# Performance work log

Measured on AMD Instinct MI355X. Metric: run time of the kernel, lower is better.

The kernel has to match this reference:

```python
import jax, jax.numpy as jnp
import numpy as np

B, S, HID = 2, 2048, 1024
H, HKV, D = 8, 2, 256
G = H // HKV            # GQA group size = 4
RD = D // 4             # partial rotary dim = 64
BASE = 10000000.0
EPS = 1e-6


def _rmsnorm(x, w):
    # x: [..., D]; matches QwenRMSNorm (fp32 math)
    xf = x.astype(jnp.float32)
    var = jnp.mean(xf * xf, axis=-1, keepdims=True)
    return w * (xf * jax.lax.rsqrt(var + EPS)).astype(x.dtype)


def _rotate_half(x):
    h = x.shape[-1] // 2
    return jnp.concatenate([-x[..., h:], x[..., :h]], axis=-1)


def _rope_cos_sin(position_ids, dtype):
    inv_freq = 1.0 / (BASE ** (jnp.arange(0, RD, 2, dtype=jnp.float32) / RD))
    freqs = position_ids.astype(jnp.float32)[:, None] * inv_freq[None, :]  # [S, RD/2]
    emb = jnp.concatenate([freqs, freqs], axis=-1)                          # [S, RD]
    return jnp.cos(emb).astype(dtype)[None, None], jnp.sin(emb).astype(dtype)[None, None]


def setup_inputs() -> dict:
    key = jax.random.key(0)
    ks = jax.random.split(key, 8)
    sc = lambda fan_in: 1.0 / np.sqrt(fan_in)
    return {
        "hidden_states": jax.random.normal(ks[0], (B, S, HID), jnp.float32),
        "position_ids": jnp.arange(S, dtype=jnp.int32),
        "Wq": jax.random.normal(ks[1], (H * D * 2, HID), jnp.float32) * sc(HID),
        "Wk": jax.random.normal(ks[2], (HKV * D, HID), jnp.float32) * sc(HID),
        "Wv": jax.random.normal(ks[3], (HKV * D, HID), jnp.float32) * sc(HID),
        "Wo": jax.random.normal(ks[4], (HID, H * D), jnp.float32) * sc(H * D),
        "q_norm_w": jnp.ones((D,), jnp.float32),
        "k_norm_w": jnp.ones((D,), jnp.float32),
    }


def reference(hidden_states, position_ids, Wq, Wk, Wv, Wo, q_norm_w, k_norm_w):
    b, s, _ = hidden_states.shape
    q_and_gate = hidden_states @ Wq.T                      # [B,S,2*H*D]
    q = q_and_gate[..., : H * D]
    gate = q_and_gate[..., H * D :]
    k = hidden_states @ Wk.T                               # [B,S,HKV*D]
    v = hidden_states @ Wv.T

    q = _rmsnorm(q.reshape(b, s, H, D), q_norm_w).transpose(0, 2, 1, 3)    # [B,H,S,D]
    k = _rmsnorm(k.reshape(b, s, HKV, D), k_norm_w).transpose(0, 2, 1, 3)  # [B,HKV,S,D]
    v = v.reshape(b, s, HKV, D).transpose(0, 2, 1, 3)                       # [B,HKV,S,D]

    cos, sin = _rope_cos_sin(position_ids, q.dtype)        # [1,1,S,RD]
    q_rot, q_pass = q[..., :RD], q[..., RD:]
    k_rot, k_pass = k[..., :RD], k[..., RD:]
    q = jnp.concatenate([q_rot * cos + _rotate_half(q_rot) * sin, q_pass], axis=-1)
    k = jnp.concatenate([k_rot * cos + _rotate_half(k_rot) * sin, k_pass], axis=-1)

    # GQA: group q heads by kv head instead of repeat_interleave (same math)
    qg = q.reshape(b, HKV, G, s, D)
    scale = 1.0 / np.sqrt(D).astype(np.float32)
    scores = jnp.einsum('bhgqd,bhkd->bhgqk', qg, k) * scale  # [B,HKV,G,S,S]
    attn = jax.nn.softmax(scores, axis=-1)                   # NOTE: no causal mask (as in source)
    out = jnp.einsum('bhgqk,bhkd->bhgqd', attn, v)           # [B,HKV,G,S,D]
    out = out.reshape(b, H, s, D).transpose(0, 2, 1, 3).reshape(b, s, H * D)

    out = out * jax.nn.silu(gate)
    return out @ Wo.T
```

## Files before the change

kernel.cpp:

```cpp
#include <hip/hip_runtime.h>
#include <math.h>

typedef unsigned short u16;
typedef unsigned int   u32;
typedef __attribute__((ext_vector_type(4))) float f32x4;
typedef __attribute__((ext_vector_type(8))) short s16x8;
typedef __attribute__((ext_vector_type(4))) unsigned short u16x4;

#define B_N   2
#define S_N   2048
#define HID_N 1024
#define H_N   8
#define HKV_N 2
#define D_N   256
#define QKVW  5120

__device__ __forceinline__ u16 f2bf(float f) {
  union { float f; u32 u; } x; x.f = f;
  u32 r = x.u + 0x7FFFu + ((x.u >> 16) & 1u);
  return (u16)(r >> 16);
}
__device__ __forceinline__ float bf2f(u16 u) {
  union { u32 u; float f; } x; x.u = ((u32)u) << 16; return x.f;
}
__device__ __forceinline__ u32 pk_bf16(float lo, float hi) {
  u32 r;
  asm("v_cvt_pk_bf16_f32 %0, %1, %2" : "=v"(r) : "v"(lo), "v"(hi));
  return r;
}
__device__ __forceinline__ void gload_lds16(const u16* g, u16* l) {
  __builtin_amdgcn_global_load_lds((const __attribute__((address_space(1))) u32*)g,
                                   (__attribute__((address_space(3))) u32*)l, 16, 0, 0);
}

__global__ __launch_bounds__(256)
void cast_bf16_kernel(const float* __restrict__ src, u16* __restrict__ dst, int n4) {
  int i = blockIdx.x * blockDim.x + threadIdx.x;
  int stride = gridDim.x * blockDim.x;
  for (; i < n4; i += stride) {
    float4 v = reinterpret_cast<const float4*>(src)[i];
    u16x4 o;
    o.x = f2bf(v.x); o.y = f2bf(v.y); o.z = f2bf(v.z); o.w = f2bf(v.w);
    reinterpret_cast<u16x4*>(dst)[i] = o;
  }
}

__global__ __launch_bounds__(256)
void trig_kernel(const int* __restrict__ pos, float* __restrict__ ct, float* __restrict__ st) {
  int i = blockIdx.x * blockDim.x + threadIdx.x;
  if (i >= S_N * 32) return;
  int s = i >> 5, j = i & 31;
  double inv = exp(-(double)j * (log(1.0e7) / 32.0));
  double ang = (double)pos[s] * inv;
  ct[i] = (float)cos(ang);
  st[i] = (float)sin(ang);
}

template <int OUT_BF16>
__global__ __launch_bounds__(256, 2)
void gemm_bt_kernel(const u16* __restrict__ A, const u16* __restrict__ Bw,
                    void* __restrict__ Cout, int M, int N, int K) {
  const int nbn = N >> 7;
  const int bm = blockIdx.x / nbn;
  const int bn = blockIdx.x % nbn;
  const int tid = threadIdx.x;
  const int lane = tid & 63;
  const int wr = tid >> 7;
  const int wc = (tid >> 6) & 1;
  __shared__ u16 sA[2][128 * 32];
  __shared__ u16 sB[2][128 * 32];
  f32x4 acc[4][4] = {};
  const u16* Ab = A + (size_t)(bm << 7) * K;
  const u16* Bb = Bw + (size_t)(bn << 7) * K;
  const int r_st = tid >> 2;
  const int c_st = (tid & 3) * 8;
  const int nkt = K >> 5;

  auto stage = [&](int buf, int kt) {
    const int k0 = kt << 5;
    gload_lds16(Ab + (size_t)r_st * K + k0 + c_st,        &sA[buf][tid * 8]);
    gload_lds16(Ab + (size_t)(r_st + 64) * K + k0 + c_st, &sA[buf][2048 + tid * 8]);
    gload_lds16(Bb + (size_t)r_st * K + k0 + c_st,        &sB[buf][tid * 8]);
    gload_lds16(Bb + (size_t)(r_st + 64) * K + k0 + c_st, &sB[buf][2048 + tid * 8]);
  };

  stage(0, 0);
  int cur = 0;
  const int ra = (wr << 6) + (lane & 15);
  const int rb = (wc << 6) + (lane & 15);
  const int ks = (lane >> 4) << 3;
  for (int kt = 0; kt < nkt; ++kt) {
    if (kt + 1 < nkt) {
      stage(cur ^ 1, kt + 1);
      asm volatile("s_waitcnt vmcnt(4)" ::: "memory");
    } else {
      asm volatile("s_waitcnt vmcnt(0)" ::: "memory");
    }
    __builtin_amdgcn_s_barrier();
    const u16* sa = sA[cur];
    const u16* sb = sB[cur];
    s16x8 af[4], bfr[4];
#pragma unroll
    for (int m = 0; m < 4; ++m) af[m] = *reinterpret_cast<const s16x8*>(sa + (ra + m * 16) * 32 + ks);
#pragma unroll
    for (int n = 0; n < 4; ++n) bfr[n] = *reinterpret_cast<const s16x8*>(sb + (rb + n * 16) * 32 + ks);
#pragma unroll
    for (int m = 0; m < 4; ++m)
#pragma unroll
      for (int n = 0; n < 4; ++n)
        acc[m][n] = __builtin_amdgcn_mfma_f32_16x16x32_bf16(af[m], bfr[n], acc[m][n], 0, 0, 0);
    __builtin_amdgcn_s_barrier();
    cur ^= 1;
  }
  const int row0 = (bm << 7) + (wr << 6) + ((lane >> 4) << 2);
  const int col0 = (bn << 7) + (wc << 6) + (lane & 15);
#pragma unroll
  for (int m = 0; m < 4; ++m)
#pragma unroll
    for (int n = 0; n < 4; ++n)
#pragma unroll
      for (int j = 0; j < 4; ++j) {
        size_t idx = (size_t)(row0 + m * 16 + j) * N + col0 + n * 16;
        if (OUT_BF16) ((u16*)Cout)[idx] = f2bf(acc[m][n][j]);
        else          ((float*)Cout)[idx] = acc[m][n][j];
      }
}

__global__ __launch_bounds__(256)
void normrope_kernel(const u16* __restrict__ qkv, const float* __restrict__ qw,
                     const float* __restrict__ kw, const float* __restrict__ ct,
                     const float* __restrict__ st, u16* __restrict__ q_r,
                     u16* __restrict__ k_r) {
  const int lane = threadIdx.x & 63;
  const int row = blockIdx.x * 4 + (threadIdx.x >> 6);
  const int nq = B_N * S_N * H_N;
  const u16* src; u16* dst; const float* w;
  int s;
  if (row < nq) {
    int h = row & 7; int bs = row >> 3; s = bs & (S_N - 1); int b = bs >> 11;
    src = qkv + (size_t)(b * S_N + s) * QKVW + h * 256;
    dst = q_r + ((size_t)(b * H_N + h) * S_N + s) * 256;
    w = qw;
  } else {
    int r2 = row - nq;
    int h = r2 & 1; int bs = r2 >> 1; s = bs & (S_N - 1); int b = bs >> 11;
    src = qkv + (size_t)(b * S_N + s) * QKVW + 4096 + h * 256;
    dst = k_r + ((size_t)(b * HKV_N + h) * S_N + s) * 256;
    w = kw;
  }
  u16x4 xv = *reinterpret_cast<const u16x4*>(src + lane * 4);
  float x0 = bf2f(xv.x), x1 = bf2f(xv.y), x2 = bf2f(xv.z), x3 = bf2f(xv.w);
  float ss = x0 * x0 + x1 * x1 + x2 * x2 + x3 * x3;
#pragma unroll
  for (int off = 1; off < 64; off <<= 1) ss += __shfl_xor(ss, off);
  float rinv = rsqrtf(ss * (1.0f / 256.0f) + 1e-6f);
  float4 wv = *reinterpret_cast<const float4*>(w + lane * 4);
  float y[4] = { x0 * rinv * wv.x, x1 * rinv * wv.y, x2 * rinv * wv.z, x3 * rinv * wv.w };
  float p[4];
  p[0] = __shfl_xor(y[0], 8);
  p[1] = __shfl_xor(y[1], 8);
  p[2] = __shfl_xor(y[2], 8);
  p[3] = __shfl_xor(y[3], 8);
  if (lane < 16) {
    const float sgn = (lane < 8) ? -1.0f : 1.0f;
    const int jb = (lane * 4) & 31;
#pragma unroll
    for (int e = 0; e < 4; ++e) {
      float c = ct[(size_t)s * 32 + jb + e];
      float sn = st[(size_t)s * 32 + jb + e];
      y[e] = y[e] * c + sgn * p[e] * sn;
    }
  }
  u16x4 ov;
  ov.x = f2bf(y[0]); ov.y = f2bf(y[1]); ov.z = f2bf(y[2]); ov.w = f2bf(y[3]);
  *reinterpret_cast<u16x4*>(dst + lane * 4) = ov;
}

__global__ __launch_bounds__(256)
void vtrans_kernel(const u16* __restrict__ qkv, u16* __restrict__ vt) {
  const int bid = blockIdx.x;
  const int dt = bid & 3;
  const int stile = (bid >> 2) & 31;
  const int bh = bid >> 7;
  const int b = bh >> 1, kvh = bh & 1;
  __shared__ u16 tile[64][68];
  const int t = threadIdx.x;
  const u16* src = qkv + (size_t)(b * S_N + stile * 64) * QKVW + 4608 + kvh * 256 + dt * 64;
#pragma unroll
  for (int i = 0; i < 2; ++i) {
    int sl = i * 32 + (t >> 3);
    int d8 = (t & 7) * 8;
    s16x8 v = *reinterpret_cast<const s16x8*>(src + (size_t)sl * QKVW + d8);
    u16x4 lo = { (u16)v[0], (u16)v[1], (u16)v[2], (u16)v[3] };
    u16x4 hi = { (u16)v[4], (u16)v[5], (u16)v[6], (u16)v[7] };
    *reinterpret_cast<u16x4*>(&tile[sl][d8]) = lo;
    *reinterpret_cast<u16x4*>(&tile[sl][d8 + 4]) = hi;
  }
  __syncthreads();
#pragma unroll
  for (int i = 0; i < 2; ++i) {
    int dl = i * 32 + (t >> 3);
    int s8 = (t & 7) * 8;
    u16 tmp[8];
#pragma unroll
    for (int e = 0; e < 8; ++e) tmp[e] = tile[s8 + e][dl];
    u16x4 lo = { tmp[0], tmp[1], tmp[2], tmp[3] };
    u16x4 hi = { tmp[4], tmp[5], tmp[6], tmp[7] };
    u16* dstp = vt + ((size_t)(bh * 256 + dt * 64 + dl)) * S_N + stile * 64 + s8;
    *reinterpret_cast<u16x4*>(dstp) = lo;
    *reinterpret_cast<u16x4*>(dstp + 4) = hi;
  }
}

__global__ __launch_bounds__(512, 2)
void attn_kernel(const u16* __restrict__ q_r, const u16* __restrict__ k_r,
                 const u16* __restrict__ vt, const u16* __restrict__ qkv,
                 u16* __restrict__ act) {
  const int dd = blockIdx.x;
  const int xcd = dd & 7;
  const int idx = dd >> 3;
  const int combo = xcd >> 1;
  const int within = (xcd & 1) * 32 + idx;
  const int b = combo >> 1;
  const int kvh = combo & 1;
  const int h = kvh * 4 + (within >> 4);
  const int qt = within & 15;

  const int tid = threadIdx.x;
  const int lane = tid & 63;
  const int wv = tid >> 6;
  const int l15 = lane & 15;
  const int l4 = lane >> 4;

  __shared__ u16 sK[2][64 * 256];
  __shared__ u16 sVt[2][256 * 64];
  __shared__ u16 sP[8][16 * 64];

  const int q0 = qt * 128 + wv * 16;
  const u16* qb = q_r + ((size_t)(b * H_N + h) * S_N + q0) * 256;
  s16x8 qf[8];
#pragma unroll
  for (int kk = 0; kk < 8; ++kk)
    qf[kk] = *reinterpret_cast<const s16x8*>(qb + (size_t)l15 * 256 + kk * 32 + l4 * 8);

  f32x4 oacc[16] = {};
  float mrow = -1e30f;
  float lrow = 0.f;

  const u16* kbase = k_r + ((size_t)(b * HKV_N + kvh) * S_N) * 256;
  const u16* vbase = vt + ((size_t)(b * HKV_N + kvh) * 256) * S_N;

  const int krow_b = tid >> 5;
  const int kp = tid & 31;
  const int vrow_b = tid >> 3;
  const int vp = tid & 7;

  auto stageKV = [&](int buf, int step) {
    const int kv0 = step << 6;
#pragma unroll
    for (int i = 0; i < 4; ++i) {
      const int krow = i * 16 + krow_b;
      gload_lds16(kbase + (size_t)(kv0 + krow) * 256 + ((kp ^ (krow_b & 7)) << 3),
                  &sK[buf][i * 4096 + tid * 8]);
    }
#pragma unroll
    for (int i = 0; i < 4; ++i) {
      const int vrow = i * 64 + vrow_b;
      gload_lds16(vbase + (size_t)vrow * S_N + kv0 + ((vp ^ (vrow_b & 7)) << 3),
                  &sVt[buf][i * 4096 + tid * 8]);
    }
  };

  stageKV(0, 0);
  int cur = 0;
  const float scale = 0.0625f;
  const int sw = l15 & 7;
  const int swp = l15 & 14;
  for (int step = 0; step < 32; ++step) {
    asm volatile("s_waitcnt vmcnt(0)" ::: "memory");
    __builtin_amdgcn_s_barrier();
    if (step + 1 < 32) stageKV(cur ^ 1, step + 1);
    const u16* ktile = sK[cur];
    const u16* vtile = sVt[cur];

    f32x4 sacc[4] = {};
#pragma unroll
    for (int kk = 0; kk < 8; ++kk) {
      const int slot = kk * 4 + l4;
#pragma unroll
      for (int g = 0; g < 4; ++g) {
        s16x8 kf = *reinterpret_cast<const s16x8*>(
            ktile + (g * 16 + l15) * 256 + ((slot ^ sw) << 3));
        sacc[g] = __builtin_amdgcn_mfma_f32_16x16x32_bf16(kf, qf[kk], sacc[g], 0, 0, 0);
      }
    }

    float vmax = sacc[0][0];
#pragma unroll
    for (int g = 0; g < 4; ++g)
#pragma unroll
      for (int j = 0; j < 4; ++j) vmax = fmaxf(vmax, sacc[g][j]);
    vmax = fmaxf(vmax, __shfl_xor(vmax, 16));
    vmax = fmaxf(vmax, __shfl_xor(vmax, 32));
    if (__any(vmax > mrow)) {
      float mnew = fmaxf(mrow, vmax);
      float alpha = __expf((mrow - mnew) * scale);
      mrow = mnew;
      lrow *= alpha;
      float ab[4];
#pragma unroll
      for (int j = 0; j < 4; ++j) ab[j] = __shfl(alpha, l4 * 4 + j);
#pragma unroll
      for (int nf = 0; nf < 16; ++nf) {
        oacc[nf][0] *= ab[0]; oacc[nf][1] *= ab[1];
        oacc[nf][2] *= ab[2]; oacc[nf][3] *= ab[3];
      }
    }
    const float msc = mrow * scale;
    float p[16];
#pragma unroll
    for (int g = 0; g < 4; ++g)
#pragma unroll
      for (int j = 0; j < 4; ++j)
        p[g * 4 + j] = __expf(fmaf(sacc[g][j], scale, -msc));
    float r = ((p[0] + p[1]) + (p[2] + p[3])) + ((p[4] + p[5]) + (p[6] + p[7]))
            + ((p[8] + p[9]) + (p[10] + p[11])) + ((p[12] + p[13]) + (p[14] + p[15]));
    r += __shfl_xor(r, 16);
    r += __shfl_xor(r, 32);
    lrow += r;

    u16* pl = &sP[wv][0];
#pragma unroll
    for (int g = 0; g < 4; ++g) {
      u32 lo = pk_bf16(p[g * 4 + 0], p[g * 4 + 1]);
      u32 hi = pk_bf16(p[g * 4 + 2], p[g * 4 + 3]);
      union { u32 w[2]; u16x4 v; } u;
      u.w[0] = lo; u.w[1] = hi;
      *reinterpret_cast<u16x4*>(pl + l15 * 64 + (((g * 4 + l4) ^ swp) << 2)) = u.v;
    }
    asm volatile("s_waitcnt lgkmcnt(0)" ::: "memory");
    __builtin_amdgcn_sched_barrier(0);

#pragma unroll
    for (int c = 0; c < 2; ++c) {
      s16x8 paf = *reinterpret_cast<const s16x8*>(
          pl + l15 * 64 + (((c * 8 + l4 * 2) ^ swp) << 2));
#pragma unroll
      for (int nf = 0; nf < 16; ++nf) {
        s16x8 vf = *reinterpret_cast<const s16x8*>(
            vtile + (nf * 16 + l15) * 64 + (((c * 4 + l4) ^ sw) << 3));
        oacc[nf] = __builtin_amdgcn_mfma_f32_16x16x32_bf16(paf, vf, oacc[nf], 0, 0, 0);
      }
    }
    cur ^= 1;
  }

  float invl = 1.0f / lrow;
  float ib[4];
#pragma unroll
  for (int j = 0; j < 4; ++j) ib[j] = __shfl(invl, l4 * 4 + j);
#pragma unroll
  for (int nf = 0; nf < 16; ++nf) {
#pragma unroll
    for (int j = 0; j < 4; ++j) {
      const int srow = q0 + l4 * 4 + j;
      const int d = nf * 16 + l15;
      float o = oacc[nf][j] * ib[j];
      float g = bf2f(qkv[(size_t)(b * S_N + srow) * QKVW + 2048 + h * 256 + d]);
      float sg = g / (1.0f + __expf(-g));
      act[(size_t)(b * S_N + srow) * 2048 + h * 256 + d] = f2bf(o * sg);
    }
  }
}

extern "C" void kernel_launch(void* const* d_in, const int* in_sizes, int n_in,
                              void* d_out, int out_size, void* d_ws, size_t ws_size,
                              hipStream_t stream) {
  const float* hs  = (const float*)d_in[0];
  const int*   pos = (const int*)d_in[1];
  const float* Wq  = (const float*)d_in[2];
  const float* Wk  = (const float*)d_in[3];
  const float* Wv  = (const float*)d_in[4];
  const float* Wo  = (const float*)d_in[5];
  const float* qw  = (const float*)d_in[6];
  const float* kw  = (const float*)d_in[7];
  float* out = (float*)d_out;

  char* w8 = (char*)d_ws;
  u16* hs_bf   = (u16*)(w8);
  u16* wqkv_bf = (u16*)(w8 + 8388608);
  u16* wo_bf   = (u16*)(w8 + 18874368);
  u16* qkv_raw = (u16*)(w8 + 23068672);
  u16* q_r     = (u16*)(w8 + 65011712);
  u16* k_r     = (u16*)(w8 + 81788928);
  u16* vt      = (u16*)(w8 + 85983232);
  u16* act     = (u16*)(w8 + 90177536);
  float* cost  = (float*)(w8 + 106954752);
  float* sint  = (float*)(w8 + 107216896);

  auto cast_launch = [&](const float* src, u16* dst, int n) {
    int n4 = n >> 2;
    int blocks = (n4 + 255) / 256;
    if (blocks > 2048) blocks = 2048;
    cast_bf16_kernel<<<blocks, 256, 0, stream>>>(src, dst, n4);
  };
  cast_launch(hs, hs_bf, B_N * S_N * HID_N);
  cast_launch(Wq, wqkv_bf, 4096 * 1024);
  cast_launch(Wk, wqkv_bf + 4194304, 512 * 1024);
  cast_launch(Wv, wqkv_bf + 4718592, 512 * 1024);
  cast_launch(Wo, wo_bf, 1024 * 2048);

  trig_kernel<<<(S_N * 32) / 256, 256, 0, stream>>>(pos, cost, sint);

  gemm_bt_kernel<1><<<32 * 40, 256, 0, stream>>>(hs_bf, wqkv_bf, (void*)qkv_raw, 4096, 5120, 1024);

  normrope_kernel<<<(B_N * S_N * (H_N + HKV_N)) / 4, 256, 0, stream>>>(
      qkv_raw, qw, kw, cost, sint, q_r, k_r);
  vtrans_kernel<<<512, 256, 0, stream>>>(qkv_raw, vt);

  attn_kernel<<<256, 512, 0, stream>>>(q_r, k_r, vt, qkv_raw, act);

  gemm_bt_kernel<0><<<32 * 8, 256, 0, stream>>>(act, wo_bf, (void*)out, 4096, 1024, 2048);
}
```

Before: 232.4 us.

## Fuse weight casts into one kernel; widen GEMM K-tile with XOR-swizzled LDS

The five separate fp32-to-bf16 cast launches become one grid-stride kernel that picks source and destination by index range, removing launch overhead. The GEMM K-tile grows from 32 to 64, which halves the number of loop iterations and barriers and doubles LDS usage. The LDS layout is XOR-swizzled to avoid bank conflicts on fragment reads. Block indices are remapped so that consecutive blocks land on 8 column groups, likely to spread them across XCDs for better L2 locality. Doubling LDS per block could reduce occupancy.

```diff
diff --git a/kernel.cpp b/kernel.cpp
--- a/kernel.cpp
+++ b/kernel.cpp
@@ -33,15 +33,31 @@
                                    (__attribute__((address_space(3))) u32*)l, 16, 0, 0);
 }
 
+#define N4_HS 1048576
+#define N4_WQ 1048576
+#define N4_WK 131072
+#define N4_WV 131072
+#define N4_WO 524288
+#define N4_TOT (N4_HS + N4_WQ + N4_WK + N4_WV + N4_WO)
+
 __global__ __launch_bounds__(256)
-void cast_bf16_kernel(const float* __restrict__ src, u16* __restrict__ dst, int n4) {
+void cast5_kernel(const float* __restrict__ hs, const float* __restrict__ wq,
+                  const float* __restrict__ wk, const float* __restrict__ wv,
+                  const float* __restrict__ wo, u16* __restrict__ hs_bf,
+                  u16* __restrict__ wqkv_bf, u16* __restrict__ wo_bf) {
   int i = blockIdx.x * blockDim.x + threadIdx.x;
-  int stride = gridDim.x * blockDim.x;
-  for (; i < n4; i += stride) {
-    float4 v = reinterpret_cast<const float4*>(src)[i];
+  const int stride = gridDim.x * blockDim.x;
+  for (; i < N4_TOT; i += stride) {
+    const float* src; u16* dst; int k;
+    if (i < N4_HS)                         { src = hs; dst = hs_bf; k = i; }
+    else if (i < N4_HS + N4_WQ)            { src = wq; dst = wqkv_bf; k = i - N4_HS; }
+    else if (i < N4_HS + N4_WQ + N4_WK)    { src = wk; dst = wqkv_bf + 4194304; k = i - (N4_HS + N4_WQ); }
+    else if (i < N4_TOT - N4_WO)           { src = wv; dst = wqkv_bf + 4718592; k = i - (N4_HS + N4_WQ + N4_WK); }
+    else                                   { src = wo; dst = wo_bf; k = i - (N4_TOT - N4_WO); }
+    float4 v = reinterpret_cast<const float4*>(src)[k];
     u16x4 o;
     o.x = f2bf(v.x); o.y = f2bf(v.y); o.z = f2bf(v.z); o.w = f2bf(v.w);
-    reinterpret_cast<u16x4*>(dst)[i] = o;
+    reinterpret_cast<u16x4*>(dst)[k] = o;
   }
 }
 
@@ -59,56 +75,70 @@
 template <int OUT_BF16>
 __global__ __launch_bounds__(256, 2)
 void gemm_bt_kernel(const u16* __restrict__ A, const u16* __restrict__ Bw,
-                    void* __restrict__ Cout, int M, int N, int K) {
-  const int nbn = N >> 7;
-  const int bm = blockIdx.x / nbn;
-  const int bn = blockIdx.x % nbn;
+                    void* __restrict__ Cout, int M, int N, int K, int bn_per_x) {
+  const int x = blockIdx.x & 7;
+  const int i0 = blockIdx.x >> 3;
+  const int bm = i0 / bn_per_x;
+  const int bn = x * bn_per_x + (i0 - bm * bn_per_x);
   const int tid = threadIdx.x;
   const int lane = tid & 63;
   const int wr = tid >> 7;
   const int wc = (tid >> 6) & 1;
-  __shared__ u16 sA[2][128 * 32];
-  __shared__ u16 sB[2][128 * 32];
+  __shared__ u16 sA[2][128 * 64];
+  __shared__ u16 sB[2][128 * 64];
   f32x4 acc[4][4] = {};
   const u16* Ab = A + (size_t)(bm << 7) * K;
   const u16* Bb = Bw + (size_t)(bn << 7) * K;
-  const int r_st = tid >> 2;
-  const int c_st = (tid & 3) * 8;
-  const int nkt = K >> 5;
+  const int nkt = K >> 6;
 
   auto stage = [&](int buf, int kt) {
-    const int k0 = kt << 5;
-    gload_lds16(Ab + (size_t)r_st * K + k0 + c_st,        &sA[buf][tid * 8]);
-    gload_lds16(Ab + (size_t)(r_st + 64) * K + k0 + c_st, &sA[buf][2048 + tid * 8]);
-    gload_lds16(Bb + (size_t)r_st * K + k0 + c_st,        &sB[buf][tid * 8]);
-    gload_lds16(Bb + (size_t)(r_st + 64) * K + k0 + c_st, &sB[buf][2048 + tid * 8]);
+    const int k0 = kt << 6;
+#pragma unroll
+    for (int i = 0; i < 4; ++i) {
+      const int L = i * 256 + tid;
+      const int r = L >> 3, s = L & 7;
+      gload_lds16(Ab + (size_t)r * K + k0 + ((s ^ (r & 7)) << 3), &sA[buf][L * 8]);
+    }
+#pragma unroll
+    for (int i = 0; i < 4; ++i) {
+      const int L = i * 256 + tid;
+      const int r = L >> 3, s = L & 7;
+      gload_lds16(Bb + (size_t)r * K + k0 + ((s ^ (r & 7)) << 3), &sB[buf][L * 8]);
+    }
   };
 
   stage(0, 0);
   int cur = 0;
   const int ra = (wr << 6) + (lane & 15);
   const int rb = (wc << 6) + (lane & 15);
-  const int ks = (lane >> 4) << 3;
+  const int l4 = (lane >> 4);
+  const int sw = lane & 7;
   for (int kt = 0; kt < nkt; ++kt) {
     if (kt + 1 < nkt) {
       stage(cur ^ 1, kt + 1);
-      asm volatile("s_waitcnt vmcnt(4)" ::: "memory");
+      asm volatile("s_waitcnt vmcnt(8)" ::: "memory");
     } else {
       asm volatile("s_waitcnt vmcnt(0)" ::: "memory");
     }
     __builtin_amdgcn_s_barrier();
     const u16* sa = sA[cur];
     const u16* sb = sB[cur];
-    s16x8 af[4], bfr[4];
-#pragma unroll
-    for (int m = 0; m < 4; ++m) af[m] = *reinterpret_cast<const s16x8*>(sa + (ra + m * 16) * 32 + ks);
-#pragma unroll
-    for (int n = 0; n < 4; ++n) bfr[n] = *reinterpret_cast<const s16x8*>(sb + (rb + n * 16) * 32 + ks);
-#pragma unroll
-    for (int m = 0; m < 4; ++m)
+#pragma unroll
+    for (int kk = 0; kk < 2; ++kk) {
+      const int sl = ((kk * 4 + l4) ^ sw) << 3;
+      s16x8 af[4], bfr[4];
+#pragma unroll
+      for (int m = 0; m < 4; ++m)
+        af[m] = *reinterpret_cast<const s16x8*>(sa + (ra + m * 16) * 64 + sl);
 #pragma unroll
       for (int n = 0; n < 4; ++n)
-        acc[m][n] = __builtin_amdgcn_mfma_f32_16x16x32_bf16(af[m], bfr[n], acc[m][n], 0, 0, 0);
+        bfr[n] = *reinterpret_cast<const s16x8*>(sb + (rb + n * 16) * 64 + sl);
+#pragma unroll
+      for (int m = 0; m < 4; ++m)
+#pragma unroll
+        for (int n = 0; n < 4; ++n)
+          acc[m][n] = __builtin_amdgcn_mfma_f32_16x16x32_bf16(af[m], bfr[n], acc[m][n], 0, 0, 0);
+    }
     __builtin_amdgcn_s_barrier();
     cur ^= 1;
   }
@@ -398,21 +428,12 @@
   float* cost  = (float*)(w8 + 106954752);
   float* sint  = (float*)(w8 + 107216896);
 
-  auto cast_launch = [&](const float* src, u16* dst, int n) {
-    int n4 = n >> 2;
-    int blocks = (n4 + 255) / 256;
-    if (blocks > 2048) blocks = 2048;
-    cast_bf16_kernel<<<blocks, 256, 0, stream>>>(src, dst, n4);
-  };
-  cast_launch(hs, hs_bf, B_N * S_N * HID_N);
-  cast_launch(Wq, wqkv_bf, 4096 * 1024);
-  cast_launch(Wk, wqkv_bf + 4194304, 512 * 1024);
-  cast_launch(Wv, wqkv_bf + 4718592, 512 * 1024);
-  cast_launch(Wo, wo_bf, 1024 * 2048);
+  cast5_kernel<<<2048, 256, 0, stream>>>(hs, Wq, Wk, Wv, Wo, hs_bf, wqkv_bf, wo_bf);
 
   trig_kernel<<<(S_N * 32) / 256, 256, 0, stream>>>(pos, cost, sint);
 
-  gemm_bt_kernel<1><<<32 * 40, 256, 0, stream>>>(hs_bf, wqkv_bf, (void*)qkv_raw, 4096, 5120, 1024);
+  gemm_bt_kernel<1><<<1280, 256, 0, stream>>>(hs_bf, wqkv_bf, (void*)qkv_raw,
+                                              4096, 5120, 1024, 5);
 
   normrope_kernel<<<(B_N * S_N * (H_N + HKV_N)) / 4, 256, 0, stream>>>(
       qkv_raw, qw, kw, cost, sint, q_r, k_r);
@@ -420,5 +441,6 @@
 
   attn_kernel<<<256, 512, 0, stream>>>(q_r, k_r, vt, qkv_raw, act);
 
-  gemm_bt_kernel<0><<<32 * 8, 256, 0, stream>>>(act, wo_bf, (void*)out, 4096, 1024, 2048);
-}
+  gemm_bt_kernel<0><<<256, 256, 0, stream>>>(act, wo_bf, (void*)out,
+                                             4096, 1024, 2048, 1);
+}
```

Result: faster. 220.8 us (-5.0%).
